# Kernel optimization log

Measured on AMD Instinct MI355X. Metric: run time of the kernel, lower is better.

## Reference

```python
import jax, jax.numpy as jnp
import numpy as np

SPLINE_ORDER = 3


def _bspline_basis(x, knots, k, order):
    """Cox-de Boor recursion with static (python float) knots, matching the torch code exactly."""
    if order == 0:
        if k + 1 >= len(knots):
            return jnp.zeros_like(x)
        return ((knots[k] <= x) & (x < knots[k + 1])).astype(x.dtype)
    left = 0.0
    right = 0.0
    if k + order < len(knots) and knots[k + order] != knots[k]:
        left = (x - knots[k]) / (knots[k + order] - knots[k]) * _bspline_basis(x, knots, k, order - 1)
    if k + order + 1 < len(knots) and knots[k + order + 1] != knots[k + 1]:
        right = (knots[k + order + 1] - x) / (knots[k + order + 1] - knots[k + 1]) * _bspline_basis(x, knots, k + 1, order - 1)
    return left + right


def setup_inputs() -> dict:
    key = jax.random.key(0)
    k1, k2, k3 = jax.random.split(key, 3)
    B, S, IN, OUT, NUM_KNOTS = 16, 4096, 256, 256, 5
    x = jax.random.normal(k1, (B, S, IN), dtype=jnp.float32)
    inner_coeffs = jax.random.normal(k2, (IN, NUM_KNOTS), dtype=jnp.float32) * 0.1
    outer_coeffs = jax.random.normal(k3, (OUT, IN), dtype=jnp.float32) * 0.1
    return {"x": x, "inner_coeffs": inner_coeffs, "outer_coeffs": outer_coeffs}


def reference(x, inner_coeffs, outer_coeffs):
    in_dim, num_knots = inner_coeffs.shape
    # knots = linspace(-1, 1, num_knots + spline_order), static python floats
    knots = np.linspace(-1.0, 1.0, num_knots + SPLINE_ORDER).tolist()
    xt = jnp.tanh(x)  # [B, S, I]
    # Original loops k in range(num_knots - spline_order); remaining basis columns stay zero,
    # so only the first n_active inner coefficients contribute.
    n_active = num_knots - SPLINE_ORDER
    basis = jnp.stack(
        [_bspline_basis(xt, knots, k, SPLINE_ORDER) for k in range(n_active)], axis=-1
    )  # [B, S, I, n_active]
    inner = jnp.einsum('bsik,ik->bsi', basis, inner_coeffs[:, :n_active])  # [B, S, I]
    return jnp.einsum('bsi,oi->bso', inner, outer_coeffs)  # [B, S, O]
```

## Files before the change

### kernel.cpp

```cpp
#include <hip/hip_runtime.h>
#include <hip/hip_bf16.h>
#include <stdint.h>


typedef __attribute__((ext_vector_type(8))) short short8;
typedef __attribute__((ext_vector_type(4))) float f32x4;

__device__ __forceinline__ uint16_t f2bf(float f) {
    union { float f; uint32_t u; } v; v.f = f;
    uint32_t r = v.u + 0x7FFFu + ((v.u >> 16) & 1u);
    return (uint16_t)(r >> 16);
}

__device__ __forceinline__ float cube_relu(float v) {
    float m = fmaxf(v, 0.0f);
    return m * m * m;
}

__device__ __forceinline__ float inner_eval(float xx, float c0, float c1) {
    float e  = __expf(2.0f * xx);
    float t  = 1.0f - 2.0f * __builtin_amdgcn_rcpf(e + 1.0f);
    float u  = (t + 1.0f) * 3.5f;
    float w0 = cube_relu(u);
    float w1 = cube_relu(u - 1.0f);
    float w2 = cube_relu(u - 2.0f);
    float w3 = cube_relu(u - 3.0f);
    float w4 = cube_relu(u - 4.0f);
    float w5 = cube_relu(u - 5.0f);
    float B0 = w0 - 4.0f*w1 + 6.0f*w2 - 4.0f*w3 + w4;
    float B1 = w1 - 4.0f*w2 + 6.0f*w3 - 4.0f*w4 + w5;
    return (c0 * B0 + c1 * B1) * (1.0f / 6.0f);
}

__device__ __forceinline__ void load_lds16(const void* g, void* l) {
    __builtin_amdgcn_global_load_lds(
        (const __attribute__((address_space(1))) uint32_t*)g,
        (__attribute__((address_space(3))) uint32_t*)l, 16, 0, 0);
}

__global__ void conv_w(const float4* __restrict__ wf, uint2* __restrict__ o) {
    const int i = blockIdx.x * blockDim.x + threadIdx.x;
    const float4 v = wf[i];
    uint2 r;
    r.x = (uint32_t)f2bf(v.x) | ((uint32_t)f2bf(v.y) << 16);
    r.y = (uint32_t)f2bf(v.z) | ((uint32_t)f2bf(v.w) << 16);
    o[i] = r;
}

#define SMEM_BYTES 22528

__global__ void kan_fused(const float* __restrict__ x,
                          const float* __restrict__ ic,
                          const uint16_t* __restrict__ wb,
                          float* __restrict__ out)
{
    __shared__ __align__(16) char smem[SMEM_BYTES];
    uint16_t* A_lds  = (uint16_t*)smem;
    char*     B_base = smem + 4096;
    float2*   C2     = (float2*)(smem + 20480);

    const int t    = threadIdx.x;
    const int lane = t & 63;
    const int w    = t >> 6;
    const int m0   = blockIdx.x * 64;

    C2[t] = make_float2(ic[t * 5 + 0], ic[t * 5 + 1]);

    f32x4 acc[4][4];
    #pragma unroll
    for (int i = 0; i < 4; ++i)
        #pragma unroll
        for (int j = 0; j < 4; ++j)
            acc[i][j] = (f32x4){0.f, 0.f, 0.f, 0.f};

    const int rowA = t >> 3;
    const int colA = (t & 7) << 2;
    const int mrow = lane & 15;
    const int quad = lane >> 4;

    #pragma unroll 1
    for (int kk = 0; kk < 8; ++kk) {
        __syncthreads();

        #pragma unroll
        for (int j = 0; j < 4; ++j) {
            const int f = ((w * 4 + j) << 10) + lane * 16;
            const int r = f >> 6;
            const int q = (f >> 4) & 3;
            load_lds16(wb + r * 256 + kk * 32 + q * 8, B_base + f);
        }

        #pragma unroll
        for (int j = 0; j < 2; ++j) {
            const int r  = rowA + j * 32;
            const int gk = kk * 32 + colA;
            const float4 xv = *(const float4*)(x + (size_t)(m0 + r) * 256 + gk);
            const float4 cA = *(const float4*)(&C2[gk]);
            const float4 cB = *(const float4*)(&C2[gk + 2]);
            float v0 = inner_eval(xv.x, cA.x, cA.y);
            float v1 = inner_eval(xv.y, cA.z, cA.w);
            float v2 = inner_eval(xv.z, cB.x, cB.y);
            float v3 = inner_eval(xv.w, cB.z, cB.w);
            uint32_t p0 = (uint32_t)f2bf(v0) | ((uint32_t)f2bf(v1) << 16);
            uint32_t p1 = (uint32_t)f2bf(v2) | ((uint32_t)f2bf(v3) << 16);
            *(uint2*)((char*)A_lds + (r * 32 + colA) * 2) = make_uint2(p0, p1);
        }

        __syncthreads();

        short8 a[4], b[4];
        #pragma unroll
        for (int i = 0; i < 4; ++i) {
            a[i] = *(const short8*)((const char*)A_lds + ((i * 16 + mrow) * 32 + quad * 8) * 2);
            b[i] = *(const short8*)(B_base + ((w * 64 + i * 16 + mrow) * 32 + quad * 8) * 2);
        }
        #pragma unroll
        for (int i = 0; i < 4; ++i)
            #pragma unroll
            for (int j = 0; j < 4; ++j)
                acc[i][j] = __builtin_amdgcn_mfma_f32_16x16x32_bf16(a[i], b[j], acc[i][j], 0, 0, 0);
    }

    #pragma unroll
    for (int i = 0; i < 4; ++i) {
        #pragma unroll
        for (int r = 0; r < 4; ++r) {
            const size_t row = (size_t)(m0 + i * 16 + quad * 4 + r);
            float* orow = out + row * 256 + w * 64 + mrow;
            #pragma unroll
            for (int j = 0; j < 4; ++j)
                orow[j * 16] = acc[i][j][r];
        }
    }
}

extern "C" void kernel_launch(void* const* d_in, const int* in_sizes, int n_in,
                              void* d_out, int out_size, void* d_ws, size_t ws_size,
                              hipStream_t stream) {
    const float* x  = (const float*)d_in[0];
    const float* ic = (const float*)d_in[1];
    const float* oc = (const float*)d_in[2];
    uint16_t* wb = (uint16_t*)d_ws;

    conv_w<<<64, 256, 0, stream>>>((const float4*)oc, (uint2*)wb);
    kan_fused<<<1024, 256, 0, stream>>>(x, ic, wb, (float*)d_out);
}
```

Measured before the change: 140.0 us.

## Double-buffer A tile, prefetch x, and load B fragments directly from global

Restructures the main loop into a software pipeline. The bf16 A tile is double-buffered in LDS so the next k-slice's spline evaluation overlaps the current MFMA block, and x is prefetched two iterations ahead into registers. B fragments are now read directly from global memory (L2-resident weights) into registers instead of staged through LDS with global_load_lds. Each iteration then needs one barrier instead of two, and LDS use drops. The custom barrier waits only on lgkmcnt, so B fragment global loads may still be in flight across it; it relies on compiler-inserted vmcnt waits before the MFMAs.

```diff
diff --git a/kernel.cpp b/kernel.cpp
--- a/kernel.cpp
+++ b/kernel.cpp
@@ -32,11 +32,12 @@
     return (c0 * B0 + c1 * B1) * (1.0f / 6.0f);
 }
 
-__device__ __forceinline__ void load_lds16(const void* g, void* l) {
-    __builtin_amdgcn_global_load_lds(
-        (const __attribute__((address_space(1))) uint32_t*)g,
-        (__attribute__((address_space(3))) uint32_t*)l, 16, 0, 0);
-}
+#define LGKM_BARRIER() do { \
+    __asm__ volatile("" ::: "memory"); \
+    __builtin_amdgcn_s_waitcnt(0xC07F); \
+    __builtin_amdgcn_s_barrier(); \
+    __asm__ volatile("" ::: "memory"); \
+} while (0)
 
 __global__ void conv_w(const float4* __restrict__ wf, uint2* __restrict__ o) {
     const int i = blockIdx.x * blockDim.x + threadIdx.x;
@@ -47,7 +48,7 @@
     o[i] = r;
 }
 
-#define SMEM_BYTES 22528
+#define SMEM_BYTES 10240
 
 __global__ void kan_fused(const float* __restrict__ x,
                           const float* __restrict__ ic,
@@ -55,16 +56,24 @@
                           float* __restrict__ out)
 {
     __shared__ __align__(16) char smem[SMEM_BYTES];
-    uint16_t* A_lds  = (uint16_t*)smem;
-    char*     B_base = smem + 4096;
-    float2*   C2     = (float2*)(smem + 20480);
+    float2* C2 = (float2*)(smem + 8192);
 
     const int t    = threadIdx.x;
     const int lane = t & 63;
     const int w    = t >> 6;
     const int m0   = blockIdx.x * 64;
+    const int rowA = t >> 3;
+    const int colA = (t & 7) << 2;
+    const int mrow = lane & 15;
+    const int quad = lane >> 4;
 
     C2[t] = make_float2(ic[t * 5 + 0], ic[t * 5 + 1]);
+
+    const float* xp0 = x + (size_t)(m0 + rowA) * 256 + colA;
+    const float* xp1 = xp0 + 32 * 256;
+
+    float4 xv0 = *(const float4*)(xp0);
+    float4 xv1 = *(const float4*)(xp1);
 
     f32x4 acc[4][4];
     #pragma unroll
@@ -73,52 +82,70 @@
         for (int j = 0; j < 4; ++j)
             acc[i][j] = (f32x4){0.f, 0.f, 0.f, 0.f};
 
-    const int rowA = t >> 3;
-    const int colA = (t & 7) << 2;
-    const int mrow = lane & 15;
-    const int quad = lane >> 4;
+    LGKM_BARRIER();
+
+    {
+        const int gk = colA;
+        const float4 cA = *(const float4*)(&C2[gk]);
+        const float4 cB = *(const float4*)(&C2[gk + 2]);
+        uint32_t p0 = (uint32_t)f2bf(inner_eval(xv0.x, cA.x, cA.y)) |
+                      ((uint32_t)f2bf(inner_eval(xv0.y, cA.z, cA.w)) << 16);
+        uint32_t p1 = (uint32_t)f2bf(inner_eval(xv0.z, cB.x, cB.y)) |
+                      ((uint32_t)f2bf(inner_eval(xv0.w, cB.z, cB.w)) << 16);
+        *(uint2*)(smem + (rowA * 32 + colA) * 2) = make_uint2(p0, p1);
+        uint32_t q0 = (uint32_t)f2bf(inner_eval(xv1.x, cA.x, cA.y)) |
+                      ((uint32_t)f2bf(inner_eval(xv1.y, cA.z, cA.w)) << 16);
+        uint32_t q1 = (uint32_t)f2bf(inner_eval(xv1.z, cB.x, cB.y)) |
+                      ((uint32_t)f2bf(inner_eval(xv1.w, cB.z, cB.w)) << 16);
+        *(uint2*)(smem + ((rowA + 32) * 32 + colA) * 2) = make_uint2(q0, q1);
+    }
+    xv0 = *(const float4*)(xp0 + 32);
+    xv1 = *(const float4*)(xp1 + 32);
 
     #pragma unroll 1
     for (int kk = 0; kk < 8; ++kk) {
-        __syncthreads();
+        const int p = kk & 1;
 
+        short8 bfrag[4];
         #pragma unroll
-        for (int j = 0; j < 4; ++j) {
-            const int f = ((w * 4 + j) << 10) + lane * 16;
-            const int r = f >> 6;
-            const int q = (f >> 4) & 3;
-            load_lds16(wb + r * 256 + kk * 32 + q * 8, B_base + f);
+        for (int j = 0; j < 4; ++j)
+            bfrag[j] = *(const short8*)(wb + (w * 64 + j * 16 + mrow) * 256 + kk * 32 + quad * 8);
+
+        LGKM_BARRIER();
+
+        short8 afrag[4];
+        const uint16_t* Ab = (const uint16_t*)(smem + p * 4096);
+        #pragma unroll
+        for (int i = 0; i < 4; ++i)
+            afrag[i] = *(const short8*)(Ab + (i * 16 + mrow) * 32 + quad * 8);
+
+        if (kk < 7) {
+            const float4 xc0 = xv0, xc1 = xv1;
+            if (kk < 6) {
+                xv0 = *(const float4*)(xp0 + (kk + 2) * 32);
+                xv1 = *(const float4*)(xp1 + (kk + 2) * 32);
+            }
+            const int gk = (kk + 1) * 32 + colA;
+            const float4 cA = *(const float4*)(&C2[gk]);
+            const float4 cB = *(const float4*)(&C2[gk + 2]);
+            char* Aw = smem + (p ^ 1) * 4096;
+            uint32_t p0 = (uint32_t)f2bf(inner_eval(xc0.x, cA.x, cA.y)) |
+                          ((uint32_t)f2bf(inner_eval(xc0.y, cA.z, cA.w)) << 16);
+            uint32_t p1 = (uint32_t)f2bf(inner_eval(xc0.z, cB.x, cB.y)) |
+                          ((uint32_t)f2bf(inner_eval(xc0.w, cB.z, cB.w)) << 16);
+            *(uint2*)(Aw + (rowA * 32 + colA) * 2) = make_uint2(p0, p1);
+            uint32_t q0 = (uint32_t)f2bf(inner_eval(xc1.x, cA.x, cA.y)) |
+                          ((uint32_t)f2bf(inner_eval(xc1.y, cA.z, cA.w)) << 16);
+            uint32_t q1 = (uint32_t)f2bf(inner_eval(xc1.z, cB.x, cB.y)) |
+                          ((uint32_t)f2bf(inner_eval(xc1.w, cB.z, cB.w)) << 16);
+            *(uint2*)(Aw + ((rowA + 32) * 32 + colA) * 2) = make_uint2(q0, q1);
         }
 
-        #pragma unroll
-        for (int j = 0; j < 2; ++j) {
-            const int r  = rowA + j * 32;
-            const int gk = kk * 32 + colA;
-            const float4 xv = *(const float4*)(x + (size_t)(m0 + r) * 256 + gk);
-            const float4 cA = *(const float4*)(&C2[gk]);
-            const float4 cB = *(const float4*)(&C2[gk + 2]);
-            float v0 = inner_eval(xv.x, cA.x, cA.y);
-            float v1 = inner_eval(xv.y, cA.z, cA.w);
-            float v2 = inner_eval(xv.z, cB.x, cB.y);
-            float v3 = inner_eval(xv.w, cB.z, cB.w);
-            uint32_t p0 = (uint32_t)f2bf(v0) | ((uint32_t)f2bf(v1) << 16);
-            uint32_t p1 = (uint32_t)f2bf(v2) | ((uint32_t)f2bf(v3) << 16);
-            *(uint2*)((char*)A_lds + (r * 32 + colA) * 2) = make_uint2(p0, p1);
-        }
-
-        __syncthreads();
-
-        short8 a[4], b[4];
-        #pragma unroll
-        for (int i = 0; i < 4; ++i) {
-            a[i] = *(const short8*)((const char*)A_lds + ((i * 16 + mrow) * 32 + quad * 8) * 2);
-            b[i] = *(const short8*)(B_base + ((w * 64 + i * 16 + mrow) * 32 + quad * 8) * 2);
-        }
         #pragma unroll
         for (int i = 0; i < 4; ++i)
             #pragma unroll
             for (int j = 0; j < 4; ++j)
-                acc[i][j] = __builtin_amdgcn_mfma_f32_16x16x32_bf16(a[i], b[j], acc[i][j], 0, 0, 0);
+                acc[i][j] = __builtin_amdgcn_mfma_f32_16x16x32_bf16(afrag[i], bfrag[j], acc[i][j], 0, 0, 0);
     }
 
     #pragma unroll
```

New measurement: 203.0 us. +45.0%, slower.

## Stage half of bf16 weights in swizzled LDS, compute A fragments in registers

Applied to the files above, without the earlier changes.

The fused KAN kernel now loads half of the bf16 outer weight matrix (256x128) into XOR-swizzled LDS at a time, refilling it once midway. Each wave evaluates the spline basis directly into its MFMA A operand registers, which removes the per-k-step A staging through LDS and the two barriers per iteration. x loads are software-prefetched one k-step ahead. The inner coefficients are pre-scaled by 1/6 in the conversion kernel, and the tanh/affine math is folded into one fma. In exchange, each wave recomputes the basis for the whole 64-row tile, so spline evaluation is duplicated 4x across waves, and the 64KB of LDS limits occupancy to 2 blocks per CU.

```diff
diff --git a/kernel.cpp b/kernel.cpp
--- a/kernel.cpp
+++ b/kernel.cpp
@@ -19,8 +19,8 @@
 
 __device__ __forceinline__ float inner_eval(float xx, float c0, float c1) {
     float e  = __expf(2.0f * xx);
-    float t  = 1.0f - 2.0f * __builtin_amdgcn_rcpf(e + 1.0f);
-    float u  = (t + 1.0f) * 3.5f;
+    float r  = __builtin_amdgcn_rcpf(e + 1.0f);
+    float u  = fmaf(-7.0f, r, 7.0f);
     float w0 = cube_relu(u);
     float w1 = cube_relu(u - 1.0f);
     float w2 = cube_relu(u - 2.0f);
@@ -29,42 +29,69 @@
     float w5 = cube_relu(u - 5.0f);
     float B0 = w0 - 4.0f*w1 + 6.0f*w2 - 4.0f*w3 + w4;
     float B1 = w1 - 4.0f*w2 + 6.0f*w3 - 4.0f*w4 + w5;
-    return (c0 * B0 + c1 * B1) * (1.0f / 6.0f);
+    return fmaf(c0, B0, c1 * B1);
 }
 
-__device__ __forceinline__ void load_lds16(const void* g, void* l) {
-    __builtin_amdgcn_global_load_lds(
-        (const __attribute__((address_space(1))) uint32_t*)g,
-        (__attribute__((address_space(3))) uint32_t*)l, 16, 0, 0);
-}
+#define LGKM_BARRIER() do { \
+    __asm__ volatile("" ::: "memory"); \
+    __builtin_amdgcn_s_waitcnt(0xC07F); \
+    __builtin_amdgcn_s_barrier(); \
+    __asm__ volatile("" ::: "memory"); \
+} while (0)
 
-__global__ void conv_w(const float4* __restrict__ wf, uint2* __restrict__ o) {
+__global__ void conv_w(const float4* __restrict__ wf, uint2* __restrict__ o,
+                       const float* __restrict__ ic, float2* __restrict__ ct) {
     const int i = blockIdx.x * blockDim.x + threadIdx.x;
     const float4 v = wf[i];
     uint2 r;
     r.x = (uint32_t)f2bf(v.x) | ((uint32_t)f2bf(v.y) << 16);
     r.y = (uint32_t)f2bf(v.z) | ((uint32_t)f2bf(v.w) << 16);
     o[i] = r;
+    if (blockIdx.x == 0) {
+        const int t = threadIdx.x;
+        ct[t] = make_float2(ic[t * 5 + 0] * (1.0f / 6.0f), ic[t * 5 + 1] * (1.0f / 6.0f));
+    }
 }
 
-#define SMEM_BYTES 22528
-
-__global__ void kan_fused(const float* __restrict__ x,
-                          const float* __restrict__ ic,
-                          const uint16_t* __restrict__ wb,
-                          float* __restrict__ out)
+__global__ __launch_bounds__(256, 2)
+void kan_fused(const float* __restrict__ x,
+               const float2* __restrict__ ct,
+               const uint16_t* __restrict__ wb,
+               float* __restrict__ out)
 {
-    __shared__ __align__(16) char smem[SMEM_BYTES];
-    uint16_t* A_lds  = (uint16_t*)smem;
-    char*     B_base = smem + 4096;
-    float2*   C2     = (float2*)(smem + 20480);
+    __shared__ uint16_t Wlds[256 * 128];
 
     const int t    = threadIdx.x;
     const int lane = t & 63;
     const int w    = t >> 6;
     const int m0   = blockIdx.x * 64;
+    const int mrow = lane & 15;
+    const int quad = lane >> 4;
+    const int nw   = w * 64;
 
-    C2[t] = make_float2(ic[t * 5 + 0], ic[t * 5 + 1]);
+    const float4* ctf4 = (const float4*)ct;
+
+    const float* xr0 = x + (size_t)(m0 + mrow) * 256 + quad * 8;
+
+    int wboff[4];
+    #pragma unroll
+    for (int j = 0; j < 4; ++j) wboff[j] = (nw + j * 16 + mrow) * 128;
+
+    float4 xa[4], xb[4];
+    #pragma unroll
+    for (int i = 0; i < 4; ++i) {
+        const float* p = xr0 + i * 16 * 256;
+        xa[i] = *(const float4*)(p);
+        xb[i] = *(const float4*)(p + 4);
+    }
+
+    #pragma unroll
+    for (int rep = 0; rep < 16; ++rep) {
+        const int flat = rep * 256 + t;
+        const int n = flat >> 4, c = flat & 15;
+        short8 v = *(const short8*)(wb + n * 256 + c * 8);
+        *(short8*)(&Wlds[n * 128 + ((c ^ (n & 15)) << 3)]) = v;
+    }
 
     f32x4 acc[4][4];
     #pragma unroll
@@ -73,52 +100,66 @@
         for (int j = 0; j < 4; ++j)
             acc[i][j] = (f32x4){0.f, 0.f, 0.f, 0.f};
 
-    const int rowA = t >> 3;
-    const int colA = (t & 7) << 2;
-    const int mrow = lane & 15;
-    const int quad = lane >> 4;
+    LGKM_BARRIER();
 
     #pragma unroll 1
     for (int kk = 0; kk < 8; ++kk) {
-        __syncthreads();
+        if (kk == 4) {
+            LGKM_BARRIER();
+            #pragma unroll
+            for (int rep = 0; rep < 16; ++rep) {
+                const int flat = rep * 256 + t;
+                const int n = flat >> 4, c = flat & 15;
+                short8 v = *(const short8*)(wb + n * 256 + 128 + c * 8);
+                *(short8*)(&Wlds[n * 128 + ((c ^ (n & 15)) << 3)]) = v;
+            }
+            LGKM_BARRIER();
+        }
+        const int kloc = kk & 3;
 
+        float4 nxa[4], nxb[4];
+        if (kk < 7) {
+            #pragma unroll
+            for (int i = 0; i < 4; ++i) {
+                const float* p = xr0 + i * 16 * 256 + (kk + 1) * 32;
+                nxa[i] = *(const float4*)(p);
+                nxb[i] = *(const float4*)(p + 4);
+            }
+        }
+
+        float4 cf[4];
         #pragma unroll
-        for (int j = 0; j < 4; ++j) {
-            const int f = ((w * 4 + j) << 10) + lane * 16;
-            const int r = f >> 6;
-            const int q = (f >> 4) & 3;
-            load_lds16(wb + r * 256 + kk * 32 + q * 8, B_base + f);
+        for (int u = 0; u < 4; ++u) cf[u] = ctf4[kk * 16 + quad * 4 + u];
+
+        short8 bf[4];
+        {
+            const int cbase = kloc * 4 + quad;
+            #pragma unroll
+            for (int j = 0; j < 4; ++j)
+                bf[j] = *(const short8*)(&Wlds[wboff[j] + ((cbase ^ mrow) << 3)]);
         }
 
         #pragma unroll
-        for (int j = 0; j < 2; ++j) {
-            const int r  = rowA + j * 32;
-            const int gk = kk * 32 + colA;
-            const float4 xv = *(const float4*)(x + (size_t)(m0 + r) * 256 + gk);
-            const float4 cA = *(const float4*)(&C2[gk]);
-            const float4 cB = *(const float4*)(&C2[gk + 2]);
-            float v0 = inner_eval(xv.x, cA.x, cA.y);
-            float v1 = inner_eval(xv.y, cA.z, cA.w);
-            float v2 = inner_eval(xv.z, cB.x, cB.y);
-            float v3 = inner_eval(xv.w, cB.z, cB.w);
-            uint32_t p0 = (uint32_t)f2bf(v0) | ((uint32_t)f2bf(v1) << 16);
-            uint32_t p1 = (uint32_t)f2bf(v2) | ((uint32_t)f2bf(v3) << 16);
-            *(uint2*)((char*)A_lds + (r * 32 + colA) * 2) = make_uint2(p0, p1);
+        for (int i = 0; i < 4; ++i) {
+            uint32_t p0 = (uint32_t)f2bf(inner_eval(xa[i].x, cf[0].x, cf[0].y)) |
+                          ((uint32_t)f2bf(inner_eval(xa[i].y, cf[0].z, cf[0].w)) << 16);
+            uint32_t p1 = (uint32_t)f2bf(inner_eval(xa[i].z, cf[1].x, cf[1].y)) |
+                          ((uint32_t)f2bf(inner_eval(xa[i].w, cf[1].z, cf[1].w)) << 16);
+            uint32_t p2 = (uint32_t)f2bf(inner_eval(xb[i].x, cf[2].x, cf[2].y)) |
+                          ((uint32_t)f2bf(inner_eval(xb[i].y, cf[2].z, cf[2].w)) << 16);
+            uint32_t p3 = (uint32_t)f2bf(inner_eval(xb[i].z, cf[3].x, cf[3].y)) |
+                          ((uint32_t)f2bf(inner_eval(xb[i].w, cf[3].z, cf[3].w)) << 16);
+            union { uint32_t u[4]; short8 s; } af;
+            af.u[0] = p0; af.u[1] = p1; af.u[2] = p2; af.u[3] = p3;
+            #pragma unroll
+            for (int j = 0; j < 4; ++j)
+                acc[i][j] = __builtin_amdgcn_mfma_f32_16x16x32_bf16(af.s, bf[j], acc[i][j], 0, 0, 0);
         }
 
-        __syncthreads();
-
-        short8 a[4], b[4];
-        #pragma unroll
-        for (int i = 0; i < 4; ++i) {
-            a[i] = *(const short8*)((const char*)A_lds + ((i * 16 + mrow) * 32 + quad * 8) * 2);
-            b[i] = *(const short8*)(B_base + ((w * 64 + i * 16 + mrow) * 32 + quad * 8) * 2);
+        if (kk < 7) {
+            #pragma unroll
+            for (int i = 0; i < 4; ++i) { xa[i] = nxa[i]; xb[i] = nxb[i]; }
         }
-        #pragma unroll
-        for (int i = 0; i < 4; ++i)
-            #pragma unroll
-            for (int j = 0; j < 4; ++j)
-                acc[i][j] = __builtin_amdgcn_mfma_f32_16x16x32_bf16(a[i], b[j], acc[i][j], 0, 0, 0);
     }
 
     #pragma unroll
@@ -126,7 +167,7 @@
         #pragma unroll
         for (int r = 0; r < 4; ++r) {
             const size_t row = (size_t)(m0 + i * 16 + quad * 4 + r);
-            float* orow = out + row * 256 + w * 64 + mrow;
+            float* orow = out + row * 256 + nw + mrow;
             #pragma unroll
             for (int j = 0; j < 4; ++j)
                 orow[j * 16] = acc[i][j][r];
@@ -140,8 +181,10 @@
     const float* x  = (const float*)d_in[0];
     const float* ic = (const float*)d_in[1];
     const float* oc = (const float*)d_in[2];
+
     uint16_t* wb = (uint16_t*)d_ws;
+    float2*   ct = (float2*)((char*)d_ws + 131072);
 
-    conv_w<<<64, 256, 0, stream>>>((const float4*)oc, (uint2*)wb);
-    kan_fused<<<1024, 256, 0, stream>>>(x, ic, wb, (float*)d_out);
+    conv_w<<<64, 256, 0, stream>>>((const float4*)oc, (uint2*)wb, ic, ct);
+    kan_fused<<<1024, 256, 0, stream>>>(x, ct, wb, (float*)d_out);
 }
```

Result: slower. 282.1 us (+101.5%).

## Drop LDS staging; pre-swizzle weights into MFMA fragment layout and read from registers

Applied to the files above, without the earlier changes.

The preprocessing kernel now writes bf16 weights already arranged in MFMA B-fragment order, and folds the 1/6 scale into the inner coefficients. The main kernel drops shared memory and barriers: each wave owns 16 rows across all 256 outputs, computes its A fragment directly in registers, and loads B fragments from global/L2. x is prefetched one K-step ahead and occupancy is pinned at 2 waves per EU. This removes LDS traffic and syncs, but every wave re-reads the full weight tile from cache and holds a larger accumulator set in registers.

```diff
diff --git a/kernel.cpp b/kernel.cpp
--- a/kernel.cpp
+++ b/kernel.cpp
@@ -1,5 +1,4 @@
 #include <hip/hip_runtime.h>
-#include <hip/hip_bf16.h>
 #include <stdint.h>
 
 
@@ -19,8 +18,8 @@
 
 __device__ __forceinline__ float inner_eval(float xx, float c0, float c1) {
     float e  = __expf(2.0f * xx);
-    float t  = 1.0f - 2.0f * __builtin_amdgcn_rcpf(e + 1.0f);
-    float u  = (t + 1.0f) * 3.5f;
+    float r  = __builtin_amdgcn_rcpf(e + 1.0f);
+    float u  = fmaf(-7.0f, r, 7.0f);
     float w0 = cube_relu(u);
     float w1 = cube_relu(u - 1.0f);
     float w2 = cube_relu(u - 2.0f);
@@ -29,108 +28,90 @@
     float w5 = cube_relu(u - 5.0f);
     float B0 = w0 - 4.0f*w1 + 6.0f*w2 - 4.0f*w3 + w4;
     float B1 = w1 - 4.0f*w2 + 6.0f*w3 - 4.0f*w4 + w5;
-    return (c0 * B0 + c1 * B1) * (1.0f / 6.0f);
+    return fmaf(c0, B0, c1 * B1);
 }
 
-__device__ __forceinline__ void load_lds16(const void* g, void* l) {
-    __builtin_amdgcn_global_load_lds(
-        (const __attribute__((address_space(1))) uint32_t*)g,
-        (__attribute__((address_space(3))) uint32_t*)l, 16, 0, 0);
+__global__ void conv_w(const float* __restrict__ oc, const float* __restrict__ ic,
+                       short8* __restrict__ wb2, float2* __restrict__ ct) {
+    const int g = blockIdx.x * 256 + threadIdx.x;
+    const int mrow = g & 15, quad = (g >> 4) & 3, jn = (g >> 6) & 15, kk = g >> 10;
+    const int n = jn * 16 + mrow, kb = kk * 32 + quad * 8;
+    const float* src = oc + n * 256 + kb;
+    const float4 u0 = *(const float4*)(src);
+    const float4 u1 = *(const float4*)(src + 4);
+    short8 v;
+    v[0] = (short)f2bf(u0.x); v[1] = (short)f2bf(u0.y);
+    v[2] = (short)f2bf(u0.z); v[3] = (short)f2bf(u0.w);
+    v[4] = (short)f2bf(u1.x); v[5] = (short)f2bf(u1.y);
+    v[6] = (short)f2bf(u1.z); v[7] = (short)f2bf(u1.w);
+    wb2[g] = v;
+    if (g < 256)
+        ct[g] = make_float2(ic[g * 5 + 0] * (1.0f / 6.0f), ic[g * 5 + 1] * (1.0f / 6.0f));
 }
 
-__global__ void conv_w(const float4* __restrict__ wf, uint2* __restrict__ o) {
-    const int i = blockIdx.x * blockDim.x + threadIdx.x;
-    const float4 v = wf[i];
-    uint2 r;
-    r.x = (uint32_t)f2bf(v.x) | ((uint32_t)f2bf(v.y) << 16);
-    r.y = (uint32_t)f2bf(v.z) | ((uint32_t)f2bf(v.w) << 16);
-    o[i] = r;
-}
-
-#define SMEM_BYTES 22528
-
-__global__ void kan_fused(const float* __restrict__ x,
-                          const float* __restrict__ ic,
-                          const uint16_t* __restrict__ wb,
-                          float* __restrict__ out)
+__global__ __launch_bounds__(256) __attribute__((amdgpu_waves_per_eu(2, 2)))
+void kan_fused(const float* __restrict__ x, const float4* __restrict__ ctf4,
+               const short8* __restrict__ wb2, float* __restrict__ out)
 {
-    __shared__ __align__(16) char smem[SMEM_BYTES];
-    uint16_t* A_lds  = (uint16_t*)smem;
-    char*     B_base = smem + 4096;
-    float2*   C2     = (float2*)(smem + 20480);
-
     const int t    = threadIdx.x;
     const int lane = t & 63;
-    const int w    = t >> 6;
+    const int mw   = t >> 6;
+    const int mrow = lane & 15;
+    const int quad = lane >> 4;
     const int m0   = blockIdx.x * 64;
 
-    C2[t] = make_float2(ic[t * 5 + 0], ic[t * 5 + 1]);
+    const float* xrow = x + (size_t)(m0 + mw * 16 + mrow) * 256 + quad * 8;
+    const short8* bbase = wb2 + quad * 16 + mrow;
 
-    f32x4 acc[4][4];
+    f32x4 acc[16];
     #pragma unroll
-    for (int i = 0; i < 4; ++i)
-        #pragma unroll
-        for (int j = 0; j < 4; ++j)
-            acc[i][j] = (f32x4){0.f, 0.f, 0.f, 0.f};
+    for (int j = 0; j < 16; ++j) acc[j] = (f32x4){0.f, 0.f, 0.f, 0.f};
 
-    const int rowA = t >> 3;
-    const int colA = (t & 7) << 2;
-    const int mrow = lane & 15;
-    const int quad = lane >> 4;
+    float4 xa = *(const float4*)(xrow);
+    float4 xb = *(const float4*)(xrow + 4);
 
     #pragma unroll 1
     for (int kk = 0; kk < 8; ++kk) {
-        __syncthreads();
+        const short8* bp = bbase + kk * 1024;
+        short8 b[16];
+        #pragma unroll
+        for (int j = 0; j < 16; ++j) b[j] = bp[j * 64];
+
+        float4 nxa, nxb;
+        if (kk < 7) {
+            const float* p = xrow + (kk + 1) * 32;
+            nxa = *(const float4*)(p);
+            nxb = *(const float4*)(p + 4);
+        }
+
+        const float4 cf0 = ctf4[kk * 16 + quad * 4 + 0];
+        const float4 cf1 = ctf4[kk * 16 + quad * 4 + 1];
+        const float4 cf2 = ctf4[kk * 16 + quad * 4 + 2];
+        const float4 cf3 = ctf4[kk * 16 + quad * 4 + 3];
+
+        short8 a;
+        a[0] = (short)f2bf(inner_eval(xa.x, cf0.x, cf0.y));
+        a[1] = (short)f2bf(inner_eval(xa.y, cf0.z, cf0.w));
+        a[2] = (short)f2bf(inner_eval(xa.z, cf1.x, cf1.y));
+        a[3] = (short)f2bf(inner_eval(xa.w, cf1.z, cf1.w));
+        a[4] = (short)f2bf(inner_eval(xb.x, cf2.x, cf2.y));
+        a[5] = (short)f2bf(inner_eval(xb.y, cf2.z, cf2.w));
+        a[6] = (short)f2bf(inner_eval(xb.z, cf3.x, cf3.y));
+        a[7] = (short)f2bf(inner_eval(xb.w, cf3.z, cf3.w));
 
         #pragma unroll
-        for (int j = 0; j < 4; ++j) {
-            const int f = ((w * 4 + j) << 10) + lane * 16;
-            const int r = f >> 6;
-            const int q = (f >> 4) & 3;
-            load_lds16(wb + r * 256 + kk * 32 + q * 8, B_base + f);
-        }
+        for (int j = 0; j < 16; ++j)
+            acc[j] = __builtin_amdgcn_mfma_f32_16x16x32_bf16(a, b[j], acc[j], 0, 0, 0);
 
-        #pragma unroll
-        for (int j = 0; j < 2; ++j) {
-            const int r  = rowA + j * 32;
-            const int gk = kk * 32 + colA;
-            const float4 xv = *(const float4*)(x + (size_t)(m0 + r) * 256 + gk);
-            const float4 cA = *(const float4*)(&C2[gk]);
-            const float4 cB = *(const float4*)(&C2[gk + 2]);
-            float v0 = inner_eval(xv.x, cA.x, cA.y);
-            float v1 = inner_eval(xv.y, cA.z, cA.w);
-            float v2 = inner_eval(xv.z, cB.x, cB.y);
-            float v3 = inner_eval(xv.w, cB.z, cB.w);
-            uint32_t p0 = (uint32_t)f2bf(v0) | ((uint32_t)f2bf(v1) << 16);
-            uint32_t p1 = (uint32_t)f2bf(v2) | ((uint32_t)f2bf(v3) << 16);
-            *(uint2*)((char*)A_lds + (r * 32 + colA) * 2) = make_uint2(p0, p1);
-        }
-
-        __syncthreads();
-
-        short8 a[4], b[4];
-        #pragma unroll
-        for (int i = 0; i < 4; ++i) {
-            a[i] = *(const short8*)((const char*)A_lds + ((i * 16 + mrow) * 32 + quad * 8) * 2);
-            b[i] = *(const short8*)(B_base + ((w * 64 + i * 16 + mrow) * 32 + quad * 8) * 2);
-        }
-        #pragma unroll
-        for (int i = 0; i < 4; ++i)
-            #pragma unroll
-            for (int j = 0; j < 4; ++j)
-                acc[i][j] = __builtin_amdgcn_mfma_f32_16x16x32_bf16(a[i], b[j], acc[i][j], 0, 0, 0);
+        if (kk < 7) { xa = nxa; xb = nxb; }
     }
 
+    const int mbase = m0 + mw * 16 + quad * 4;
     #pragma unroll
-    for (int i = 0; i < 4; ++i) {
+    for (int j = 0; j < 16; ++j) {
         #pragma unroll
-        for (int r = 0; r < 4; ++r) {
-            const size_t row = (size_t)(m0 + i * 16 + quad * 4 + r);
-            float* orow = out + row * 256 + w * 64 + mrow;
-            #pragma unroll
-            for (int j = 0; j < 4; ++j)
-                orow[j * 16] = acc[i][j][r];
-        }
+        for (int r = 0; r < 4; ++r)
+            out[(size_t)(mbase + r) * 256 + j * 16 + mrow] = acc[j][r];
     }
 }
 
@@ -140,8 +121,10 @@
     const float* x  = (const float*)d_in[0];
     const float* ic = (const float*)d_in[1];
     const float* oc = (const float*)d_in[2];
-    uint16_t* wb = (uint16_t*)d_ws;
 
-    conv_w<<<64, 256, 0, stream>>>((const float4*)oc, (uint2*)wb);
-    kan_fused<<<1024, 256, 0, stream>>>(x, ic, wb, (float*)d_out);
+    short8* wb2 = (short8*)d_ws;
+    float2* ct  = (float2*)((char*)d_ws + 131072);
+
+    conv_w<<<32, 256, 0, stream>>>(oc, ic, wb2, ct);
+    kan_fused<<<1024, 256, 0, stream>>>(x, (const float4*)ct, wb2, (float*)d_out);
 }
```

Result: slower. 159.7 us (+14.0%).
